# Kernel tuning notes

Hardware: AMD Instinct MI355X
Metric: run time of the kernel (lower is better)

The kernel has to match this reference:

```python
import jax, jax.numpy as jnp
import numpy as np

B, N, C_Z, H, C_H, W = 1, 192, 128, 4, 32, 16


def _layer_norm(x, w, b, eps=1e-5):
    mu = jnp.mean(x, axis=-1, keepdims=True)
    var = jnp.mean(jnp.square(x - mu), axis=-1, keepdims=True)
    return (x - mu) * jax.lax.rsqrt(var + eps) * w + b


def setup_inputs() -> dict:
    key = jax.random.key(0)
    ks = jax.random.split(key, 10)
    s = 0.02
    return {
        "z": jax.random.normal(ks[0], (B, N, N, C_Z), jnp.float32),
        "mask": jnp.ones((B, N, N), jnp.float32),
        "ln_w": jnp.ones((C_Z,), jnp.float32),
        "ln_b": jnp.zeros((C_Z,), jnp.float32),
        "w_q": jax.random.normal(ks[1], (C_Z, H * C_H), jnp.float32) * s,
        "w_k": jax.random.normal(ks[2], (C_Z, H * C_H), jnp.float32) * s,
        "w_v": jax.random.normal(ks[3], (C_Z, H * C_H), jnp.float32) * s,
        "w_bias": jax.random.normal(ks[4], (C_Z, H), jnp.float32) * s,
        "w_gate": jax.random.normal(ks[5], (C_Z, H * C_H), jnp.float32) * s,
        "b_gate": jnp.ones((H * C_H,), jnp.float32),
        "w_out": jax.random.normal(ks[6], (H * C_H, C_Z), jnp.float32) * s,
        "b_out": jnp.zeros((C_Z,), jnp.float32),
        "window_size": W,
    }


def reference(z, mask, ln_w, ln_b, w_q, w_k, w_v, w_bias, w_gate, b_gate, w_out, b_out, window_size):
    b, n = z.shape[0], z.shape[1]
    h = w_bias.shape[1]
    c = w_q.shape[1] // h
    w = int(window_size)

    zl = _layer_norm(z, ln_w, ln_b)                       # [B,N,N,Cz]
    q = (zl @ w_q).reshape(b, n, n, h, c)                 # [B,I,J,H,c]
    k = (zl @ w_k).reshape(b, n, n, h, c)
    v = (zl @ w_v).reshape(b, n, n, h, c)
    tb = zl @ w_bias                                      # [B,J,K,H] triangle bias

    # sliding window indices along the key axis, centered at each query j
    idx = jnp.arange(n)[:, None] - (w // 2) + jnp.arange(w)[None, :]   # [N,W]
    valid = (idx >= 0) & (idx < n)                                     # [N,W]
    idx_c = jnp.clip(idx, 0, n - 1)

    k_win = k[:, :, idx_c]                                # [B,I,J,W,H,c]
    v_win = v[:, :, idx_c]                                # [B,I,J,W,H,c]
    tb_win = jnp.take_along_axis(tb, idx_c[None, :, :, None], axis=2)  # [B,J,W,H]
    mask_win = mask[:, :, idx_c] * valid[None, None].astype(mask.dtype)  # [B,I,J,W]

    scale = 1.0 / jnp.sqrt(jnp.asarray(c, z.dtype))
    logits = jnp.einsum('bijhc,bijwhc->bijwh', q * scale, k_win)       # [B,I,J,W,H]
    logits = logits + tb_win[:, None]                                  # bias b_{j,k} broadcast over i
    logits = logits + jnp.where(mask_win > 0, 0.0, -1e9)[..., None]
    attn = jax.nn.softmax(logits, axis=3)

    o = jnp.einsum('bijwh,bijwhc->bijhc', attn, v_win)                 # [B,I,J,H,c]
    g = jax.nn.sigmoid(zl @ w_gate + b_gate).reshape(b, n, n, h, c)
    o = (g * o).reshape(b, n, n, h * c)
    return o @ w_out + b_out                                           # [B,I,J,Cz]
```

## Files before the change

### kernel.cpp

```cpp
#include <hip/hip_runtime.h>
#include <hip/hip_bf16.h>

#define N 192
#define CZ 128
#define NH 4
#define CH 32
#define WIN 16
#define NROWS (N*N)

typedef __attribute__((ext_vector_type(8))) short bf16x8;
typedef __attribute__((ext_vector_type(4))) float f32x4;

static __device__ __forceinline__ ushort f2bf(float x){
    union{float f; unsigned u;} a; a.f = x;
    unsigned r = a.u + 0x7fffu + ((a.u>>16)&1u);
    return (ushort)(r>>16);
}
static __device__ __forceinline__ float bf2f(ushort s){
    union{unsigned u; float f;} a; a.u = ((unsigned)s)<<16;
    return a.f;
}

__global__ __launch_bounds__(256) void k_tb_pack(
    const float* __restrict__ z, const float* __restrict__ lnw, const float* __restrict__ lnb,
    const float* __restrict__ wbias, float* __restrict__ tb,
    const float* __restrict__ wq, const float* __restrict__ wk,
    const float* __restrict__ wv, const float* __restrict__ wg,
    const float* __restrict__ wo, ushort* __restrict__ WP)
{
    const int tid = threadIdx.x;
    if (blockIdx.x < 40) {
        const int m = blockIdx.x >> 3;
        const float* W = (m==0)?wq:(m==1)?wk:(m==2)?wv:(m==3)?wg:wo;
        const int f = (blockIdx.x & 7)*256 + tid;
        const int nt = f >> 8, ks = (f >> 6) & 3, lane8 = f & 63;
        const int col = nt*16 + (lane8 & 15);
        const int r0  = ks*32 + (lane8 >> 4)*8;
        ushort tmp[8];
        #pragma unroll
        for (int i=0; i<8; i++) tmp[i] = f2bf(W[(size_t)(r0+i)*CZ + col]);
        *(uint4*)(WP + (size_t)m*16384 + (size_t)f*8) = *(uint4*)tmp;
    }
    const int wave = tid >> 6, lane = tid & 63;
    const int r  = wave*4 + (lane >> 4);
    const int li = lane & 15;
    const int row = blockIdx.x*16 + r;
    const float* zr = z + (size_t)row*CZ + li*8;
    float4 a = ((const float4*)zr)[0];
    float4 b = ((const float4*)zr)[1];
    float s  = a.x+a.y+a.z+a.w + b.x+b.y+b.z+b.w;
    float s2 = a.x*a.x+a.y*a.y+a.z*a.z+a.w*a.w + b.x*b.x+b.y*b.y+b.z*b.z+b.w*b.w;
    #pragma unroll
    for (int off=1; off<16; off<<=1) { s += __shfl_xor(s, off); s2 += __shfl_xor(s2, off); }
    const float mu   = s * (1.f/CZ);
    const float rstd = rsqrtf(s2*(1.f/CZ) - mu*mu + 1e-5f);
    const int c0 = li*8;
    float vals[8] = {a.x,a.y,a.z,a.w,b.x,b.y,b.z,b.w};
    float tbp[4] = {0.f,0.f,0.f,0.f};
    #pragma unroll
    for (int t=0; t<8; t++) {
        const float nv = (vals[t]-mu)*rstd*lnw[c0+t] + lnb[c0+t];
        float4 wb4 = *(const float4*)(wbias + (c0+t)*4);
        tbp[0] += nv*wb4.x; tbp[1] += nv*wb4.y;
        tbp[2] += nv*wb4.z; tbp[3] += nv*wb4.w;
    }
    #pragma unroll
    for (int off=1; off<16; off<<=1) {
        #pragma unroll
        for (int h=0; h<4; h++) tbp[h] += __shfl_xor(tbp[h], off);
    }
    if (li == 0) *(float4*)(tb + (size_t)row*4) = make_float4(tbp[0],tbp[1],tbp[2],tbp[3]);
}

__global__ __launch_bounds__(256, 3) void k_fused(
    const float* __restrict__ z, const float* __restrict__ lnw, const float* __restrict__ lnb,
    const float* __restrict__ mask, const float* __restrict__ tb,
    const ushort* __restrict__ WP, const float* __restrict__ bg,
    const float* __restrict__ bout, float* __restrict__ out)
{
    __shared__ ushort zlds[48][132];
    __shared__ ushort kl[48][NH][40];
    __shared__ ushort vl[48][NH][40];
    __shared__ ushort qb[32][136];
    __shared__ float  ml[48];
    ushort (*gpo)[136] = (ushort (*)[136])&zlds[0][0];

    const int i   = blockIdx.y;
    const int j0  = blockIdx.x * 32;
    const int tid = threadIdx.x;
    const int wid = tid >> 6, lane = tid & 63;
    const int l16 = lane & 15, lk = lane >> 4;

    for (int it = 0; it < 3; ++it) {
        const int r   = it*16 + wid*4 + lk;
        const int jj  = j0 - 8 + r;
        const int jjc = min(max(jj, 0), N-1);
        const float* zr = z + ((size_t)i*N + jjc)*CZ + l16*8;
        float4 a = ((const float4*)zr)[0];
        float4 b = ((const float4*)zr)[1];
        float s  = a.x+a.y+a.z+a.w + b.x+b.y+b.z+b.w;
        float s2 = a.x*a.x+a.y*a.y+a.z*a.z+a.w*a.w + b.x*b.x+b.y*b.y+b.z*b.z+b.w*b.w;
        #pragma unroll
        for (int off=1; off<16; off<<=1) { s += __shfl_xor(s, off); s2 += __shfl_xor(s2, off); }
        const float mu   = s * (1.f/CZ);
        const float rstd = rsqrtf(s2*(1.f/CZ) - mu*mu + 1e-5f);
        const int c0 = l16*8;
        float vals[8] = {a.x,a.y,a.z,a.w,b.x,b.y,b.z,b.w};
        uint4 pk; ushort* ph = (ushort*)&pk;
        #pragma unroll
        for (int t=0; t<8; t++)
            ph[t] = f2bf((vals[t]-mu)*rstd*lnw[c0+t] + lnb[c0+t]);
        *(uint4*)&zlds[r][c0] = pk;
    }
    if (tid < 47) {
        const int jj  = j0 - 8 + tid;
        const int jjc = min(max(jj, 0), N-1);
        const bool ok = (jj >= 0) && (jj < N) && (mask[(size_t)i*N + jjc] > 0.f);
        ml[tid] = ok ? 0.f : -1e9f;
    }
    __syncthreads();

    uint2 gst0[2], gst1[2];
    {
        const int cw = wid;
        bf16x8 bfrag[2][4];
        auto loadB = [&](int m) {
            #pragma unroll
            for (int nt2=0; nt2<2; nt2++)
                #pragma unroll
                for (int ks=0; ks<4; ks++)
                    bfrag[nt2][ks] = *(const bf16x8*)(WP + (size_t)m*16384 + (cw*2+nt2)*2048 + ks*512 + lane*8);
        };
        auto projKV = [&](int slot0, ushort (*dst)[NH][40]) {
            bf16x8 af[4];
            #pragma unroll
            for (int ks=0; ks<4; ks++)
                af[ks] = *(const bf16x8*)&zlds[slot0 + l16][ks*32 + lk*8];
            #pragma unroll
            for (int nt2=0; nt2<2; nt2++) {
                f32x4 acc = {0.f,0.f,0.f,0.f};
                #pragma unroll
                for (int ks=0; ks<4; ks++)
                    acc = __builtin_amdgcn_mfma_f32_16x16x32_bf16(bfrag[nt2][ks], af[ks], acc, 0, 0, 0);
                uint2 pk2;
                pk2.x = (unsigned)f2bf(acc[0]) | ((unsigned)f2bf(acc[1])<<16);
                pk2.y = (unsigned)f2bf(acc[2]) | ((unsigned)f2bf(acc[3])<<16);
                *(uint2*)&dst[slot0 + l16][cw][nt2*16 + lk*4] = pk2;
            }
        };
        auto projQ = [&](int slot0) {
            bf16x8 af[4];
            #pragma unroll
            for (int ks=0; ks<4; ks++)
                af[ks] = *(const bf16x8*)&zlds[slot0 + l16][ks*32 + lk*8];
            #pragma unroll
            for (int nt2=0; nt2<2; nt2++) {
                f32x4 acc = {0.f,0.f,0.f,0.f};
                #pragma unroll
                for (int ks=0; ks<4; ks++)
                    acc = __builtin_amdgcn_mfma_f32_16x16x32_bf16(bfrag[nt2][ks], af[ks], acc, 0, 0, 0);
                uint2 pk2;
                pk2.x = (unsigned)f2bf(acc[0]) | ((unsigned)f2bf(acc[1])<<16);
                pk2.y = (unsigned)f2bf(acc[2]) | ((unsigned)f2bf(acc[3])<<16);
                *(uint2*)&qb[slot0 - 8 + l16][cw*32 + nt2*16 + lk*4] = pk2;
            }
        };
        auto projG = [&](int slot0, uint2* gs) {
            float4 bg4[2];
            #pragma unroll
            for (int nt2=0; nt2<2; nt2++)
                bg4[nt2] = *(const float4*)(bg + cw*32 + nt2*16 + lk*4);
            bf16x8 af[4];
            #pragma unroll
            for (int ks=0; ks<4; ks++)
                af[ks] = *(const bf16x8*)&zlds[slot0 + l16][ks*32 + lk*8];
            #pragma unroll
            for (int nt2=0; nt2<2; nt2++) {
                f32x4 acc = {0.f,0.f,0.f,0.f};
                #pragma unroll
                for (int ks=0; ks<4; ks++)
                    acc = __builtin_amdgcn_mfma_f32_16x16x32_bf16(bfrag[nt2][ks], af[ks], acc, 0, 0, 0);
                const float v0 = 1.f/(1.f + __expf(-(acc[0] + bg4[nt2].x)));
                const float v1 = 1.f/(1.f + __expf(-(acc[1] + bg4[nt2].y)));
                const float v2 = 1.f/(1.f + __expf(-(acc[2] + bg4[nt2].z)));
                const float v3 = 1.f/(1.f + __expf(-(acc[3] + bg4[nt2].w)));
                uint2 pk2;
                pk2.x = (unsigned)f2bf(v0) | ((unsigned)f2bf(v1)<<16);
                pk2.y = (unsigned)f2bf(v2) | ((unsigned)f2bf(v3)<<16);
                gs[nt2] = pk2;
            }
        };

        loadB(1); projKV(0, kl); projKV(16, kl); projKV(32, kl);
        loadB(2); projKV(0, vl); projKV(16, vl); projKV(32, vl);
        loadB(0); projQ(8);  projQ(24);
        loadB(3); projG(8, gst0); projG(24, gst1);
    }
    __syncthreads();
    {
        const int cw = wid;
        *(uint2*)&gpo[l16     ][cw*32      + lk*4] = gst0[0];
        *(uint2*)&gpo[l16     ][cw*32 + 16 + lk*4] = gst0[1];
        *(uint2*)&gpo[16 + l16][cw*32      + lk*4] = gst1[0];
        *(uint2*)&gpo[16 + l16][cw*32 + 16 + lk*4] = gst1[1];
    }
    __syncthreads();

    const int chalf = tid & 1;
    const int h     = (tid >> 1) & 3;
    const int jloc  = tid >> 3;
    const int j     = j0 + jloc;
    const int c0l   = chalf * 16;

    float qv[16];
    {
        uint4 q1 = *(const uint4*)&qb[jloc][h*CH + c0l];
        uint4 q2 = *(const uint4*)&qb[jloc][h*CH + c0l + 8];
        const ushort* s1 = (const ushort*)&q1;
        const ushort* s2 = (const ushort*)&q2;
        #pragma unroll
        for (int t=0; t<8; t++) { qv[t] = bf2f(s1[t]); qv[8+t] = bf2f(s2[t]); }
    }

    const float scale = 0.17677669529663688f;
    float lg[WIN];
    #pragma unroll
    for (int w=0; w<WIN; w++) {
        const int rel = jloc + w;
        float dot = 0.f;
        #pragma unroll
        for (int c4=0; c4<2; c4++) {
            uint4 kv = *(const uint4*)&kl[rel][h][c0l + c4*8];
            const ushort* kp = (const ushort*)&kv;
            #pragma unroll
            for (int t=0; t<8; t++) dot += qv[c4*8+t]*bf2f(kp[t]);
        }
        dot += __shfl_xor(dot, 1);
        const int jj  = j - 8 + w;
        const int jjc = min(max(jj, 0), N-1);
        lg[w] = dot*scale + tb[((size_t)j*N + jjc)*4 + h] + ml[rel];
    }
    float mx = lg[0];
    #pragma unroll
    for (int w=1; w<WIN; w++) mx = fmaxf(mx, lg[w]);
    float sum = 0.f;
    #pragma unroll
    for (int w=0; w<WIN; w++) { lg[w] = __expf(lg[w]-mx); sum += lg[w]; }
    const float inv = 1.f/sum;

    float o[16];
    #pragma unroll
    for (int c=0; c<16; c++) o[c] = 0.f;
    #pragma unroll
    for (int w=0; w<WIN; w++) {
        const float p   = lg[w]*inv;
        const int   rel = jloc + w;
        #pragma unroll
        for (int c4=0; c4<2; c4++) {
            uint4 vv = *(const uint4*)&vl[rel][h][c0l + c4*8];
            const ushort* vp = (const ushort*)&vv;
            #pragma unroll
            for (int t=0; t<8; t++) o[c4*8+t] += p*bf2f(vp[t]);
        }
    }

    {
        uint4 g1 = *(const uint4*)&gpo[jloc][h*CH + c0l];
        uint4 g2 = *(const uint4*)&gpo[jloc][h*CH + c0l + 8];
        const ushort* s1 = (const ushort*)&g1;
        const ushort* s2 = (const ushort*)&g2;
        uint4 o1, o2; ushort* p1 = (ushort*)&o1; ushort* p2 = (ushort*)&o2;
        #pragma unroll
        for (int t=0; t<8; t++) {
            p1[t] = f2bf(o[t]   * bf2f(s1[t]));
            p2[t] = f2bf(o[8+t] * bf2f(s2[t]));
        }
        *(uint4*)&gpo[jloc][h*CH + c0l]     = o1;
        *(uint4*)&gpo[jloc][h*CH + c0l + 8] = o2;
    }

    const int cwo = wid;
    bf16x8 bfrag[2][4];
    float4 bo4[2];
    #pragma unroll
    for (int nt2=0; nt2<2; nt2++) {
        #pragma unroll
        for (int ks=0; ks<4; ks++)
            bfrag[nt2][ks] = *(const bf16x8*)(WP + (size_t)4*16384 + (cwo*2+nt2)*2048 + ks*512 + lane*8);
        bo4[nt2] = *(const float4*)(bout + cwo*32 + nt2*16 + lk*4);
    }
    __syncthreads();

    #pragma unroll
    for (int rt=0; rt<2; rt++) {
        bf16x8 af[4];
        #pragma unroll
        for (int ks=0; ks<4; ks++)
            af[ks] = *(const bf16x8*)&gpo[rt*16 + l16][ks*32 + lk*8];
        const size_t orow = (size_t)(i*N + j0 + rt*16 + l16)*CZ;
        #pragma unroll
        for (int nt2=0; nt2<2; nt2++) {
            f32x4 acc = {0.f,0.f,0.f,0.f};
            #pragma unroll
            for (int ks=0; ks<4; ks++)
                acc = __builtin_amdgcn_mfma_f32_16x16x32_bf16(bfrag[nt2][ks], af[ks], acc, 0, 0, 0);
            float4 ov;
            ov.x = acc[0] + bo4[nt2].x; ov.y = acc[1] + bo4[nt2].y;
            ov.z = acc[2] + bo4[nt2].z; ov.w = acc[3] + bo4[nt2].w;
            *(float4*)(out + orow + cwo*32 + nt2*16 + lk*4) = ov;
        }
    }
}

extern "C" void kernel_launch(void* const* d_in, const int* in_sizes, int n_in,
                              void* d_out, int out_size, void* d_ws, size_t ws_size,
                              hipStream_t stream)
{
    const float* z    = (const float*)d_in[0];
    const float* mask = (const float*)d_in[1];
    const float* lnw  = (const float*)d_in[2];
    const float* lnb  = (const float*)d_in[3];
    const float* wq   = (const float*)d_in[4];
    const float* wk   = (const float*)d_in[5];
    const float* wv   = (const float*)d_in[6];
    const float* wb   = (const float*)d_in[7];
    const float* wg   = (const float*)d_in[8];
    const float* bg   = (const float*)d_in[9];
    const float* wo   = (const float*)d_in[10];
    const float* bo   = (const float*)d_in[11];

    float*  tb = (float*)d_ws;
    ushort* WP = (ushort*)(tb + (size_t)NROWS*4);
    if (ws_size < (size_t)NROWS*4*sizeof(float) + 5*16384*sizeof(ushort)) return;

    k_tb_pack<<<NROWS/16, 256, 0, stream>>>(z, lnw, lnb, wb, tb, wq, wk, wv, wg, wo, WP);
    k_fused  <<<dim3(N/32, N), 256, 0, stream>>>(z, lnw, lnb, mask, tb, WP, bg, bo, (float*)d_out);
}
```

Before: 45.37 us.

## Batch z loads, prefetch K/V and out-proj weights, move barrier past attention

All three z rows are now loaded before any LayerNorm math, so the global loads overlap instead of running one after another. The output-projection weights and bias are fetched before the attention loop instead of after it, which hides their latency behind compute. The K and V loops are software-pipelined with a one-step register prefetch from LDS. The barrier after the gate stores is moved to just before the gated-output write, so attention runs without waiting on the gate writes. This raises register pressure, which may lower occupancy, and the barrier placement has to keep the gpo accesses race-free.

Result: no change. 46.11 us (+1.6%).

```diff
diff --git a/kernel.cpp b/kernel.cpp
--- a/kernel.cpp
+++ b/kernel.cpp
@@ -91,26 +91,35 @@
     const int wid = tid >> 6, lane = tid & 63;
     const int l16 = lane & 15, lk = lane >> 4;
 
-    for (int it = 0; it < 3; ++it) {
-        const int r   = it*16 + wid*4 + lk;
-        const int jj  = j0 - 8 + r;
-        const int jjc = min(max(jj, 0), N-1);
-        const float* zr = z + ((size_t)i*N + jjc)*CZ + l16*8;
-        float4 a = ((const float4*)zr)[0];
-        float4 b = ((const float4*)zr)[1];
-        float s  = a.x+a.y+a.z+a.w + b.x+b.y+b.z+b.w;
-        float s2 = a.x*a.x+a.y*a.y+a.z*a.z+a.w*a.w + b.x*b.x+b.y*b.y+b.z*b.z+b.w*b.w;
-        #pragma unroll
-        for (int off=1; off<16; off<<=1) { s += __shfl_xor(s, off); s2 += __shfl_xor(s2, off); }
-        const float mu   = s * (1.f/CZ);
-        const float rstd = rsqrtf(s2*(1.f/CZ) - mu*mu + 1e-5f);
-        const int c0 = l16*8;
-        float vals[8] = {a.x,a.y,a.z,a.w,b.x,b.y,b.z,b.w};
-        uint4 pk; ushort* ph = (ushort*)&pk;
-        #pragma unroll
-        for (int t=0; t<8; t++)
-            ph[t] = f2bf((vals[t]-mu)*rstd*lnw[c0+t] + lnb[c0+t]);
-        *(uint4*)&zlds[r][c0] = pk;
+    {
+        float4 za[3], zb[3];
+        #pragma unroll
+        for (int it = 0; it < 3; ++it) {
+            const int r   = it*16 + wid*4 + lk;
+            const int jj  = j0 - 8 + r;
+            const int jjc = min(max(jj, 0), N-1);
+            const float* zr = z + ((size_t)i*N + jjc)*CZ + l16*8;
+            za[it] = ((const float4*)zr)[0];
+            zb[it] = ((const float4*)zr)[1];
+        }
+        #pragma unroll
+        for (int it = 0; it < 3; ++it) {
+            const int r = it*16 + wid*4 + lk;
+            float4 a = za[it], b = zb[it];
+            float s  = a.x+a.y+a.z+a.w + b.x+b.y+b.z+b.w;
+            float s2 = a.x*a.x+a.y*a.y+a.z*a.z+a.w*a.w + b.x*b.x+b.y*b.y+b.z*b.z+b.w*b.w;
+            #pragma unroll
+            for (int off=1; off<16; off<<=1) { s += __shfl_xor(s, off); s2 += __shfl_xor(s2, off); }
+            const float mu   = s * (1.f/CZ);
+            const float rstd = rsqrtf(s2*(1.f/CZ) - mu*mu + 1e-5f);
+            const int c0 = l16*8;
+            float vals[8] = {a.x,a.y,a.z,a.w,b.x,b.y,b.z,b.w};
+            uint4 pk; ushort* ph = (ushort*)&pk;
+            #pragma unroll
+            for (int t=0; t<8; t++)
+                ph[t] = f2bf((vals[t]-mu)*rstd*lnw[c0+t] + lnb[c0+t]);
+            *(uint4*)&zlds[r][c0] = pk;
+        }
     }
     if (tid < 47) {
         const int jj  = j0 - 8 + tid;
@@ -204,7 +213,6 @@
         *(uint2*)&gpo[16 + l16][cw*32      + lk*4] = gst1[0];
         *(uint2*)&gpo[16 + l16][cw*32 + 16 + lk*4] = gst1[1];
     }
-    __syncthreads();
 
     const int chalf = tid & 1;
     const int h     = (tid >> 1) & 3;
@@ -222,23 +230,46 @@
         for (int t=0; t<8; t++) { qv[t] = bf2f(s1[t]); qv[8+t] = bf2f(s2[t]); }
     }
 
+    const int cwo = wid;
+    bf16x8 bfrag[2][4];
+    float4 bo4[2];
+    #pragma unroll
+    for (int nt2=0; nt2<2; nt2++) {
+        #pragma unroll
+        for (int ks=0; ks<4; ks++)
+            bfrag[nt2][ks] = *(const bf16x8*)(WP + (size_t)4*16384 + (cwo*2+nt2)*2048 + ks*512 + lane*8);
+        bo4[nt2] = *(const float4*)(bout + cwo*32 + nt2*16 + lk*4);
+    }
+
     const float scale = 0.17677669529663688f;
     float lg[WIN];
     #pragma unroll
     for (int w=0; w<WIN; w++) {
-        const int rel = jloc + w;
-        float dot = 0.f;
-        #pragma unroll
-        for (int c4=0; c4<2; c4++) {
-            uint4 kv = *(const uint4*)&kl[rel][h][c0l + c4*8];
-            const ushort* kp = (const ushort*)&kv;
-            #pragma unroll
-            for (int t=0; t<8; t++) dot += qv[c4*8+t]*bf2f(kp[t]);
-        }
-        dot += __shfl_xor(dot, 1);
         const int jj  = j - 8 + w;
         const int jjc = min(max(jj, 0), N-1);
-        lg[w] = dot*scale + tb[((size_t)j*N + jjc)*4 + h] + ml[rel];
+        lg[w] = tb[((size_t)j*N + jjc)*4 + h] + ml[jloc + w];
+    }
+    {
+        uint4 k1 = *(const uint4*)&kl[jloc][h][c0l];
+        uint4 k2 = *(const uint4*)&kl[jloc][h][c0l + 8];
+        #pragma unroll
+        for (int w=0; w<WIN; w++) {
+            uint4 n1, n2;
+            if (w < WIN-1) {
+                n1 = *(const uint4*)&kl[jloc+w+1][h][c0l];
+                n2 = *(const uint4*)&kl[jloc+w+1][h][c0l + 8];
+            }
+            float dot = 0.f;
+            const ushort* kp1 = (const ushort*)&k1;
+            const ushort* kp2 = (const ushort*)&k2;
+            #pragma unroll
+            for (int t=0; t<8; t++) dot += qv[t]*bf2f(kp1[t]);
+            #pragma unroll
+            for (int t=0; t<8; t++) dot += qv[8+t]*bf2f(kp2[t]);
+            dot += __shfl_xor(dot, 1);
+            lg[w] += dot*scale;
+            k1 = n1; k2 = n2;
+        }
     }
     float mx = lg[0];
     #pragma unroll
@@ -251,18 +282,27 @@
     float o[16];
     #pragma unroll
     for (int c=0; c<16; c++) o[c] = 0.f;
-    #pragma unroll
-    for (int w=0; w<WIN; w++) {
-        const float p   = lg[w]*inv;
-        const int   rel = jloc + w;
-        #pragma unroll
-        for (int c4=0; c4<2; c4++) {
-            uint4 vv = *(const uint4*)&vl[rel][h][c0l + c4*8];
-            const ushort* vp = (const ushort*)&vv;
-            #pragma unroll
-            for (int t=0; t<8; t++) o[c4*8+t] += p*bf2f(vp[t]);
-        }
-    }
+    {
+        uint4 v1 = *(const uint4*)&vl[jloc][h][c0l];
+        uint4 v2 = *(const uint4*)&vl[jloc][h][c0l + 8];
+        #pragma unroll
+        for (int w=0; w<WIN; w++) {
+            uint4 n1, n2;
+            if (w < WIN-1) {
+                n1 = *(const uint4*)&vl[jloc+w+1][h][c0l];
+                n2 = *(const uint4*)&vl[jloc+w+1][h][c0l + 8];
+            }
+            const float p = lg[w]*inv;
+            const ushort* vp1 = (const ushort*)&v1;
+            const ushort* vp2 = (const ushort*)&v2;
+            #pragma unroll
+            for (int t=0; t<8; t++) o[t]   += p*bf2f(vp1[t]);
+            #pragma unroll
+            for (int t=0; t<8; t++) o[8+t] += p*bf2f(vp2[t]);
+            v1 = n1; v2 = n2;
+        }
+    }
+    __syncthreads();
 
     {
         uint4 g1 = *(const uint4*)&gpo[jloc][h*CH + c0l];
@@ -277,17 +317,6 @@
         }
         *(uint4*)&gpo[jloc][h*CH + c0l]     = o1;
         *(uint4*)&gpo[jloc][h*CH + c0l + 8] = o2;
-    }
-
-    const int cwo = wid;
-    bf16x8 bfrag[2][4];
-    float4 bo4[2];
-    #pragma unroll
-    for (int nt2=0; nt2<2; nt2++) {
-        #pragma unroll
-        for (int ks=0; ks<4; ks++)
-            bfrag[nt2][ks] = *(const bf16x8*)(WP + (size_t)4*16384 + (cwo*2+nt2)*2048 + ks*512 + lane*8);
-        bo4[nt2] = *(const float4*)(bout + cwo*32 + nt2*16 + lk*4);
     }
     __syncthreads();
 
```
